# Optimization experiments

Hardware: AMD Instinct MI355X
Metric: run time of the kernel (lower is better)

The kernel has to match this reference:

```python
import jax, jax.numpy as jnp
import numpy as np

DIM = 1024
SCALE = DIM ** (-0.5)
TEMPERATURE = 1.0


def setup_inputs() -> dict:
    key = jax.random.key(0)
    ks = jax.random.split(key, 7)
    B, N, D = 8, 4096, DIM
    s = 1.0 / np.sqrt(D)
    return {
        "x": jax.random.normal(ks[0], (B, N, D), dtype=jnp.float32),
        "Wq": jax.random.normal(ks[1], (D, D), dtype=jnp.float32) * s,
        "bq": jax.random.normal(ks[2], (D,), dtype=jnp.float32) * 0.01,
        "Wk": jax.random.normal(ks[3], (D, D), dtype=jnp.float32) * s,
        "bk": jax.random.normal(ks[4], (D,), dtype=jnp.float32) * 0.01,
        "Wv": jax.random.normal(ks[5], (D, D), dtype=jnp.float32) * s,
        "bv": jax.random.normal(ks[6], (D,), dtype=jnp.float32) * 0.01,
    }


def reference(x, Wq, bq, Wk, bk, Wv, bv):
    B, N, D = x.shape
    # adaptive_avg_pool1d from N -> N//2 with N even == mean over adjacent pairs
    q_input = x.reshape(B, N // 2, 2, D).mean(axis=2)  # [B, N/2, D]
    # torch Linear: y = x @ W.T + b
    q = jnp.einsum("bmd,ed->bme", q_input, Wq) + bq      # [B, N/2, D]
    k = jnp.einsum("bnd,ed->bne", x, Wk) + bk            # [B, N, D]
    v = jnp.einsum("bnd,ed->bne", x, Wv) + bv            # [B, N, D]
    attn = jnp.einsum("bmd,bnd->bmn", q, k) * SCALE      # [B, N/2, N]
    attn = jax.nn.softmax(attn * TEMPERATURE, axis=-1)
    k_out = jnp.einsum("bmn,bnd->bmd", attn, v)          # [B, N/2, D]
    return (q, k_out, k_out)
```

## Files before the change

kernel.cpp:

```cpp
#include <hip/hip_runtime.h>
#include <hip/hip_bf16.h>
#include <cstddef>

typedef __attribute__((ext_vector_type(8))) short s16x8;
typedef __attribute__((ext_vector_type(4))) short s16x4;
typedef __attribute__((ext_vector_type(4))) float f32x4;

#define MFMA_BF16(a, b, c) __builtin_amdgcn_mfma_f32_16x16x32_bf16((a), (b), (c), 0, 0, 0)

__device__ __forceinline__ short f2bf(float f) {
    union { float f; unsigned u; } cv; cv.f = f;
    unsigned u = cv.u;
    unsigned r = (u + 0x7FFFu + ((u >> 16) & 1u)) >> 16;
    return (short)r;
}
__device__ __forceinline__ float bf2f(unsigned short u) {
    union { unsigned u; float f; } cv; cv.u = ((unsigned)u) << 16; return cv.f;
}

__device__ __forceinline__ void gl16(const void* g, void* l) {
    __builtin_amdgcn_global_load_lds(
        (const __attribute__((address_space(1))) void*)g,
        (__attribute__((address_space(3))) void*)l, 16, 0, 0);
}

template <int MODE>
__global__ __launch_bounds__(256, 2) void gemm_bf(
    const void* __restrict__ Ap, const short* __restrict__ Bp,
    const float* __restrict__ bias, const float* __restrict__ lvec,
    void* __restrict__ Cp, void* __restrict__ Cp2,
    int zbase, float* __restrict__ lpart)
{
    constexpr int NT  = (MODE == 4 || MODE == 7) ? 64 : 16;
    constexpr int LDA = (MODE == 4 || MODE == 7) ? 4096 : 1024;
    constexpr int LDB = (MODE == 4 || MODE == 7) ? 4096 : 1024;

    __shared__ short As[128 * 64];
    __shared__ short Bs[128 * 64];
    const int tid = threadIdx.x;

    int bx, by, z;
    if constexpr (MODE == 6 || MODE == 7) {
        const int n = blockIdx.x;
        z = (n & 3) + zbase; const int m = n >> 2; by = m % 16; bx = m / 16;
    } else if constexpr (MODE == 1 || MODE == 3 || MODE == 4 || MODE == 5) {
        const int n = blockIdx.x;
        constexpr int NBY = (MODE == 1) ? 8 : 16;
        z = n & 7; const int m = n >> 3; by = m % NBY; bx = m / NBY;
    } else { bx = blockIdx.x; by = blockIdx.y; z = blockIdx.z; }

    const int w = tid >> 6, l = tid & 63, l15 = l & 15, lhi = l >> 4;
    const int wy = w >> 1, wx = w & 1;
    const int X = (l15 & 7) << 3;
    const int lr8 = l >> 3, cb = l & 7, scb = cb ^ lr8;

    size_t arow0 = (size_t)by * 128, brow0 = (size_t)bx * 128;
    if constexpr (MODE == 3 || MODE == 4 || MODE == 5 || MODE == 6) arow0 += (size_t)z * 2048;
    if constexpr (MODE == 7) arow0 += (size_t)(z & 3) * 2048;
    if constexpr (MODE == 1 || MODE == 3 || MODE == 5 || MODE == 6) brow0 += (size_t)z * 4096;
    if constexpr (MODE == 4 || MODE == 7) brow0 += (size_t)z * 1024;

    const short* Ab = (const short*)Ap;
    const float* Af = (const float*)Ap;

    const short* gA = Ab + (arow0 + w * 32 + lr8) * (size_t)LDA + scb * 8;
    const short* gB = Bp + (brow0 + w * 32 + lr8) * (size_t)LDB + scb * 8;

    f32x4 acc[4][4];
    #pragma unroll
    for (int m = 0; m < 4; ++m)
        #pragma unroll
        for (int n = 0; n < 4; ++n) acc[m][n] = (f32x4){0.f, 0.f, 0.f, 0.f};

    const int r0b = tid >> 3, cb8 = (tid & 7) * 8;
    const int r0f = tid >> 4, kcs = tid & 15;

    for (int kt = 0; kt < NT; ++kt) {
        #pragma unroll
        for (int i = 0; i < 4; ++i)
            gl16(gB + (size_t)(i * 8) * LDB + kt * 64, &Bs[(w * 32 + i * 8) * 64]);
        if constexpr (MODE == 2) {
            #pragma unroll
            for (int p = 0; p < 4; ++p) {
                const int r = r0b + p * 32;
                const size_t g = (arow0 + r) * 2048 + kt * 64 + cb8;
                s16x8 u0 = *(const s16x8*)(Ab + g);
                s16x8 u1 = *(const s16x8*)(Ab + g + 1024);
                s16x8 o;
                #pragma unroll
                for (int j = 0; j < 8; ++j)
                    o[j] = f2bf(0.5f * (bf2f((unsigned short)u0[j]) + bf2f((unsigned short)u1[j])));
                *(s16x8*)&As[r * 64 + (cb8 ^ ((r & 7) * 8))] = o;
            }
        } else if constexpr (MODE == 3) {
            const int k0 = kt * 64 + kcs * 4;
            #pragma unroll
            for (int p = 0; p < 8; ++p) {
                const int r = r0f + p * 16;
                float4 u = *(const float4*)(Af + (arow0 + r) * 1024 + k0);
                s16x4 sa = { f2bf(u.x * 0.03125f), f2bf(u.y * 0.03125f),
                             f2bf(u.z * 0.03125f), f2bf(u.w * 0.03125f) };
                *(s16x4*)&As[r * 64 + ((kcs * 4) ^ ((r & 7) * 8))] = sa;
            }
        } else {
            #pragma unroll
            for (int i = 0; i < 4; ++i)
                gl16(gA + (size_t)(i * 8) * LDA + kt * 64, &As[(w * 32 + i * 8) * 64]);
        }
        __syncthreads();
        #pragma unroll
        for (int kk = 0; kk < 2; ++kk) {
            const int e = (kk * 32 + lhi * 8) ^ X;
            s16x8 af[4], bfr[4];
            #pragma unroll
            for (int m = 0; m < 4; ++m)
                af[m] = *(const s16x8*)&As[(wy * 64 + m * 16 + l15) * 64 + e];
            #pragma unroll
            for (int n = 0; n < 4; ++n)
                bfr[n] = *(const s16x8*)&Bs[(wx * 64 + n * 16 + l15) * 64 + e];
            #pragma unroll
            for (int m = 0; m < 4; ++m)
                #pragma unroll
                for (int n = 0; n < 4; ++n)
                    acc[m][n] = MFMA_BF16(af[m], bfr[n], acc[m][n]);
        }
        __syncthreads();
    }

    #pragma unroll
    for (int m = 0; m < 4; ++m) {
        #pragma unroll
        for (int j = 0; j < 4; ++j) {
            const int rl = wy * 64 + m * 16 + lhi * 4 + j;
            const int grow = by * 128 + rl;
            float radd = 0.f, rmul = 1.f;
            if constexpr (MODE == 1) radd = bias[grow];
            if constexpr (MODE == 4 || MODE == 7) rmul = 1.0f / lvec[(size_t)z * 2048 + grow];
            if constexpr (MODE == 6) {
                float s = 0.f;
                #pragma unroll
                for (int n = 0; n < 4; ++n) {
                    const int gcol = bx * 128 + wx * 64 + n * 16 + l15;
                    const float pv = __expf(acc[m][n][j]);
                    s += pv;
                    ((short*)Cp)[(size_t)(z & 3) * 8388608 + (size_t)grow * 4096 + gcol] = f2bf(pv);
                }
                s += __shfl_xor(s, 1);
                s += __shfl_xor(s, 2);
                s += __shfl_xor(s, 4);
                s += __shfl_xor(s, 8);
                if (l15 == 0)
                    lpart[((size_t)(z & 3) * 2048 + grow) * 64 + bx * 2 + wx] = s;
            } else {
                #pragma unroll
                for (int n = 0; n < 4; ++n) {
                    const int cl = wx * 64 + n * 16 + l15;
                    const int gcol = bx * 128 + cl;
                    float v = acc[m][n][j];
                    if constexpr (MODE == 0) {
                        ((short*)Cp)[(size_t)grow * 1024 + gcol] = f2bf(v + bias[gcol]);
                    } else if constexpr (MODE == 1) {
                        ((short*)Cp)[(size_t)z * 4194304 + (size_t)grow * 4096 + gcol] = f2bf(v + radd);
                    } else if constexpr (MODE == 2) {
                        const float qv = v + bias[gcol];
                        ((float*)Cp)[(size_t)grow * 1024 + gcol] = qv;
                        if (Cp2 != nullptr)
                            ((short*)Cp2)[(size_t)grow * 1024 + gcol] = f2bf(qv * 0.03125f);
                    } else if constexpr (MODE == 3 || MODE == 5) {
                        ((short*)Cp)[(size_t)z * 8388608 + (size_t)grow * 4096 + gcol] = f2bf(v);
                    } else {
                        const size_t o = ((size_t)z * 2048 + grow) * 1024 + gcol;
                        const float ov = v * rmul;
                        ((float*)Cp)[o] = ov;
                        ((float*)Cp2)[o] = ov;
                    }
                }
            }
        }
    }
}

__global__ __launch_bounds__(256, 4) void reduce_l(
    const float* __restrict__ lpart, float* __restrict__ lvec, int zbase)
{
    const int r = blockIdx.x * 256 + threadIdx.x;
    const float4* p = (const float4*)(lpart + (size_t)r * 64);
    float s = 0.f;
    #pragma unroll
    for (int i = 0; i < 16; ++i) { float4 v = p[i]; s += v.x + v.y + v.z + v.w; }
    lvec[(size_t)zbase * 2048 + r] = s;
}

template <int MODE>
__global__ __launch_bounds__(256, 2) void gemm_f32(
    const float* __restrict__ Ap, const float* __restrict__ Bp,
    const float* __restrict__ bias, void* __restrict__ Cp, void* __restrict__ Cp2)
{
    constexpr int LDA = (MODE == 2) ? 2048 : 1024;
    __shared__ short As[128 * 64];
    __shared__ short Bs[128 * 64];
    const int tid = threadIdx.x;
    const int bx = blockIdx.x, by = blockIdx.y, z = blockIdx.z;
    const int w = tid >> 6, l = tid & 63, l15 = l & 15, lhi = l >> 4;
    const int wy = w >> 1, wx = w & 1;
    const int X = (l15 & 7) << 3;

    size_t arow0 = (size_t)by * 128, brow0 = (size_t)bx * 128;
    if constexpr (MODE == 1) brow0 += (size_t)z * 4096;

    f32x4 acc[4][4];
    #pragma unroll
    for (int m = 0; m < 4; ++m)
        #pragma unroll
        for (int n = 0; n < 4; ++n) acc[m][n] = (f32x4){0.f, 0.f, 0.f, 0.f};

    const int r0f = tid >> 4, kcs = tid & 15;
    float4 ra[8], ra2[8], rb[8];

    auto load_tile = [&](int kt) {
        const int k0 = kt * 64 + kcs * 4;
        #pragma unroll
        for (int p = 0; p < 8; ++p) {
            const int r = r0f + p * 16;
            if constexpr (MODE == 2) {
                const float* s0 = Ap + (arow0 + r) * (size_t)LDA + k0;
                ra[p] = *(const float4*)s0;
                ra2[p] = *(const float4*)(s0 + 1024);
            } else {
                ra[p] = *(const float4*)(Ap + (arow0 + r) * (size_t)LDA + k0);
            }
            rb[p] = *(const float4*)(Bp + (brow0 + r) * (size_t)1024 + k0);
        }
    };

    load_tile(0);
    for (int kt = 0; kt < 16; ++kt) {
        #pragma unroll
        for (int p = 0; p < 8; ++p) {
            const int r = r0f + p * 16;
            const int e = (kcs * 4) ^ ((r & 7) << 3);
            float ax, ay, az, aw;
            if constexpr (MODE == 2) {
                ax = 0.5f * (ra[p].x + ra2[p].x); ay = 0.5f * (ra[p].y + ra2[p].y);
                az = 0.5f * (ra[p].z + ra2[p].z); aw = 0.5f * (ra[p].w + ra2[p].w);
            } else {
                ax = ra[p].x; ay = ra[p].y; az = ra[p].z; aw = ra[p].w;
            }
            s16x4 sa = { f2bf(ax), f2bf(ay), f2bf(az), f2bf(aw) };
            *(s16x4*)&As[r * 64 + e] = sa;
            s16x4 sb = { f2bf(rb[p].x), f2bf(rb[p].y), f2bf(rb[p].z), f2bf(rb[p].w) };
            *(s16x4*)&Bs[r * 64 + e] = sb;
        }
        if (kt + 1 < 16) load_tile(kt + 1);
        __syncthreads();
        #pragma unroll
        for (int kk = 0; kk < 2; ++kk) {
            const int e = (kk * 32 + lhi * 8) ^ X;
            s16x8 af[4], bfr[4];
            #pragma unroll
            for (int m = 0; m < 4; ++m)
                af[m] = *(const s16x8*)&As[(wy * 64 + m * 16 + l15) * 64 + e];
            #pragma unroll
            for (int n = 0; n < 4; ++n)
                bfr[n] = *(const s16x8*)&Bs[(wx * 64 + n * 16 + l15) * 64 + e];
            #pragma unroll
            for (int m = 0; m < 4; ++m)
                #pragma unroll
                for (int n = 0; n < 4; ++n)
                    acc[m][n] = MFMA_BF16(af[m], bfr[n], acc[m][n]);
        }
        __syncthreads();
    }

    #pragma unroll
    for (int m = 0; m < 4; ++m) {
        #pragma unroll
        for (int j = 0; j < 4; ++j) {
            const int rl = wy * 64 + m * 16 + lhi * 4 + j;
            const int grow = by * 128 + rl;
            const float radd = (MODE == 1) ? bias[grow] : 0.f;
            #pragma unroll
            for (int n = 0; n < 4; ++n) {
                const int cl = wx * 64 + n * 16 + l15;
                const int gcol = bx * 128 + cl;
                float v = acc[m][n][j];
                if constexpr (MODE == 0) {
                    ((short*)Cp)[(size_t)grow * 1024 + gcol] = f2bf(v + bias[gcol]);
                } else if constexpr (MODE == 1) {
                    ((short*)Cp)[(size_t)z * 4194304 + (size_t)grow * 4096 + gcol] = f2bf(v + radd);
                } else {
                    const float q = v + bias[gcol];
                    ((float*)Cp)[(size_t)grow * 1024 + gcol] = q;
                    ((short*)Cp2)[(size_t)grow * 1024 + gcol] = f2bf(q * 0.03125f);
                }
            }
        }
    }
}

__global__ __launch_bounds__(256, 4) void convert_x(const float* __restrict__ x,
                                                    short* __restrict__ xb)
{
    const size_t i0 = ((size_t)blockIdx.x * 256 + threadIdx.x) * 8;
    float4 a = *(const float4*)(x + i0), b = *(const float4*)(x + i0 + 4);
    s16x8 o = { f2bf(a.x), f2bf(a.y), f2bf(a.z), f2bf(a.w),
                f2bf(b.x), f2bf(b.y), f2bf(b.z), f2bf(b.w) };
    *(s16x8*)(xb + i0) = o;
}

__global__ __launch_bounds__(256, 4) void convert_w(
    const float* __restrict__ Wq, const float* __restrict__ Wk,
    const float* __restrict__ Wv, short* __restrict__ Wb)
{
    const int gid = blockIdx.x * 256 + threadIdx.x;
    const int seg = gid >> 17;
    const size_t off = (size_t)(gid & 131071) * 8;
    const float* s = (seg == 0) ? Wq : ((seg == 1) ? Wk : Wv);
    float4 a = *(const float4*)(s + off), b = *(const float4*)(s + off + 4);
    s16x8 o = { f2bf(a.x), f2bf(a.y), f2bf(a.z), f2bf(a.w),
                f2bf(b.x), f2bf(b.y), f2bf(b.z), f2bf(b.w) };
    *(s16x8*)(Wb + (size_t)seg * 1048576 + off) = o;
}

__global__ __launch_bounds__(256, 4) void softmax_rows(
    const unsigned short* __restrict__ Sin, unsigned short* __restrict__ Pout,
    float* __restrict__ lvec)
{
    const int w = threadIdx.x >> 6, l = threadIdx.x & 63;
    const int row = blockIdx.x * 4 + w;
    const unsigned short* rp = Sin + (size_t)row * 4096;
    unsigned short* wp = Pout + (size_t)row * 4096;

    s16x8 v[8];
    #pragma unroll
    for (int c = 0; c < 8; ++c)
        v[c] = *(const s16x8*)(rp + (c * 64 + l) * 8);

    float mx = -1e30f;
    #pragma unroll
    for (int c = 0; c < 8; ++c)
        #pragma unroll
        for (int j = 0; j < 8; ++j)
            mx = fmaxf(mx, bf2f((unsigned short)v[c][j]));
    #pragma unroll
    for (int d = 1; d < 64; d <<= 1) mx = fmaxf(mx, __shfl_xor(mx, d));

    float sum = 0.f;
    #pragma unroll
    for (int c = 0; c < 8; ++c) {
        #pragma unroll
        for (int j = 0; j < 8; ++j) {
            const float p = __expf(bf2f((unsigned short)v[c][j]) - mx);
            sum += p;
            v[c][j] = f2bf(p);
        }
    }
    #pragma unroll
    for (int d = 1; d < 64; d <<= 1) sum += __shfl_xor(sum, d);

    #pragma unroll
    for (int c = 0; c < 8; ++c)
        *(s16x8*)(wp + (c * 64 + l) * 8) = v[c];
    if (l == 0) lvec[row] = sum;
}

__global__ __launch_bounds__(256, 4) void dup_out(
    const float4* __restrict__ O, float4* __restrict__ o1, float4* __restrict__ o2)
{
    const size_t i0 = (size_t)blockIdx.x * 256 + threadIdx.x;
    #pragma unroll
    for (int p = 0; p < 4; ++p) {
        const size_t i = i0 + (size_t)p * 1048576;
        const float4 t = O[i];
        o1[i] = t;
        o2[i] = t;
    }
}

extern "C" void kernel_launch(void* const* d_in, const int* in_sizes, int n_in,
                              void* d_out, int out_size, void* d_ws, size_t ws_size,
                              hipStream_t stream) {
    const float* x  = (const float*)d_in[0];
    const float* Wq = (const float*)d_in[1];
    const float* bq = (const float*)d_in[2];
    const float* Wk = (const float*)d_in[3];
    const float* bk = (const float*)d_in[4];
    const float* Wv = (const float*)d_in[5];
    const float* bv = (const float*)d_in[6];

    float* out   = (float*)d_out;
    float* q_out = out;
    float* out1  = out + (size_t)16777216;
    float* out2  = out + (size_t)33554432;
    short* Smat  = (short*)out1;

    const unsigned long long NEED_A2 = 241434624ULL;
    const unsigned long long NEED_A1 = 207683584ULL;

    if ((unsigned long long)ws_size >= NEED_A2) {
        short* xb  = (short*)d_ws;
        short* Wb  = xb + (size_t)33554432;
        short* kws = Wb + (size_t)3145728;
        short* vT  = kws + (size_t)33554432;
        short* qs  = vT + (size_t)33554432;
        float* lws = (float*)(qs + (size_t)16777216);
        short* Pws   = (short*)d_ws;
        float* lpart = (float*)((char*)d_ws + 67108864);

        convert_x<<<dim3(16384, 1, 1), 256, 0, stream>>>(x, xb);
        convert_w<<<dim3(1536, 1, 1), 256, 0, stream>>>(Wq, Wk, Wv, Wb);
        gemm_bf<0><<<dim3(8, 256, 1), 256, 0, stream>>>(xb, Wb + 1048576, bk, nullptr, (void*)kws, nullptr, 0, nullptr);
        gemm_bf<1><<<dim3(2048, 1, 1), 256, 0, stream>>>(Wb + 2097152, xb, bv, nullptr, (void*)vT, nullptr, 0, nullptr);
        gemm_bf<2><<<dim3(8, 128, 1), 256, 0, stream>>>(xb, Wb, bq, nullptr, (void*)q_out, (void*)qs, 0, nullptr);
        for (int half = 0; half < 2; ++half) {
            const int zb = half * 4;
            gemm_bf<6><<<dim3(2048, 1, 1), 256, 0, stream>>>(qs, kws, nullptr, nullptr, (void*)Pws, nullptr, zb, lpart);
            reduce_l<<<dim3(32, 1, 1), 256, 0, stream>>>(lpart, lws, zb);
            gemm_bf<7><<<dim3(512, 1, 1), 256, 0, stream>>>(Pws, vT, nullptr, lws, (void*)out1, (void*)out2, zb, nullptr);
        }
    } else if ((unsigned long long)ws_size >= NEED_A1) {
        short* xb  = (short*)d_ws;
        short* Wb  = xb + (size_t)33554432;
        short* kws = Wb + (size_t)3145728;
        short* vT  = kws + (size_t)33554432;
        float* lws = (float*)((char*)d_ws + 207618048ULL);
        unsigned short* Pws = (unsigned short*)d_ws;

        convert_x<<<dim3(16384, 1, 1), 256, 0, stream>>>(x, xb);
        convert_w<<<dim3(1536, 1, 1), 256, 0, stream>>>(Wq, Wk, Wv, Wb);
        gemm_bf<0><<<dim3(8, 256, 1), 256, 0, stream>>>(xb, Wb + 1048576, bk, nullptr, (void*)kws, nullptr, 0, nullptr);
        gemm_bf<1><<<dim3(2048, 1, 1), 256, 0, stream>>>(Wb + 2097152, xb, bv, nullptr, (void*)vT, nullptr, 0, nullptr);
        gemm_bf<2><<<dim3(8, 128, 1), 256, 0, stream>>>(xb, Wb, bq, nullptr, (void*)q_out, nullptr, 0, nullptr);
        gemm_bf<3><<<dim3(4096, 1, 1), 256, 0, stream>>>(q_out, kws, nullptr, nullptr, (void*)Smat, nullptr, 0, nullptr);
        softmax_rows<<<dim3(4096, 1, 1), 256, 0, stream>>>((const unsigned short*)Smat, Pws, lws);
        gemm_bf<4><<<dim3(1024, 1, 1), 256, 0, stream>>>(Pws, vT, nullptr, lws, (void*)out1, (void*)out2, 0, nullptr);
    } else {
        short* kws = (short*)d_ws;
        short* vT  = kws + (size_t)33554432;
        short* qs  = vT + (size_t)33554432;
        float* lws = (float*)((char*)d_ws + 167772160ULL);
        float* Ows = (float*)d_ws;

        gemm_f32<0><<<dim3(8, 256, 1), 256, 0, stream>>>(x, Wk, bk, (void*)kws, nullptr);
        gemm_f32<1><<<dim3(32, 8, 8), 256, 0, stream>>>(Wv, x, bv, (void*)vT, nullptr);
        gemm_f32<2><<<dim3(8, 128, 1), 256, 0, stream>>>(x, Wq, bq, (void*)q_out, (void*)qs);
        gemm_bf<5><<<dim3(4096, 1, 1), 256, 0, stream>>>(qs, kws, nullptr, nullptr, (void*)Smat, nullptr, 0, nullptr);
        softmax_rows<<<dim3(4096, 1, 1), 256, 0, stream>>>((const unsigned short*)Smat, (unsigned short*)Smat, lws);
        gemm_bf<4><<<dim3(1024, 1, 1), 256, 0, stream>>>(Smat, vT, nullptr, lws, (void*)Ows, (void*)Ows, 0, nullptr);
        dup_out<<<dim3(4096, 1, 1), 256, 0, stream>>>((const float4*)Ows, (float4*)out1, (float4*)out2);
    }
}
```

Measured before the change: 636.9 us.

## Add 256x256-tile double-buffered QK^T kernel with exp epilogue

Replaces the 128x128-tile QK^T+exp GEMM with a new 512-thread kernel computing 256x256 output tiles, double-buffered LDS staging via global_load_lds, and fragment reuse across four MFMA sub-phases with setprio. Larger tiles raise arithmetic intensity and cut global traffic per FLOP for the score matrix. The cost is heavy LDS use (128KB) and many accumulator registers, which may limit occupancy. The lpart layout must still match what reduce_l expects (64 partials per row).

```diff
diff --git a/kernel.cpp b/kernel.cpp
--- a/kernel.cpp
+++ b/kernel.cpp
@@ -22,6 +22,166 @@
     __builtin_amdgcn_global_load_lds(
         (const __attribute__((address_space(1))) void*)g,
         (__attribute__((address_space(3))) void*)l, 16, 0, 0);
+}
+
+template <int MODE>
+__global__ __launch_bounds__(512, 2) void g256(
+    const short* __restrict__ Ap, const short* __restrict__ Bp,
+    void* __restrict__ Cp, int zbase, float* __restrict__ lpart)
+{
+    constexpr int NT = 16;
+    constexpr int LDA = 1024, LDB = 1024;
+
+    __shared__ short As[2][16384];
+    __shared__ short Bs[2][16384];
+
+    const int tid = threadIdx.x;
+    const int n = blockIdx.x;
+    const int z = (n & 3) + zbase;
+    const int m_ = n >> 2;
+    const int by = m_ & 7, bx = m_ >> 3;
+    const int w = tid >> 6, l = tid & 63, l15 = l & 15, lhi = l >> 4;
+    const int wr = w >> 2, wc = w & 3;
+    const int X = (l15 & 7) << 3;
+    const int lr8 = l >> 3, cb = l & 7, scb = cb ^ lr8;
+
+    const size_t arow0 = (size_t)z * 2048 + (size_t)by * 256;
+    const size_t brow0 = (size_t)z * 4096 + (size_t)bx * 256;
+
+    const short* gA = Ap + (arow0 + w * 8 + lr8) * (size_t)LDA + scb * 8;
+    const short* gB = Bp + (brow0 + w * 8 + lr8) * (size_t)LDB + scb * 8;
+
+    f32x4 acc[8][4];
+    #pragma unroll
+    for (int mm = 0; mm < 8; ++mm)
+        #pragma unroll
+        for (int nn = 0; nn < 4; ++nn) acc[mm][nn] = (f32x4){0.f, 0.f, 0.f, 0.f};
+
+    auto STAGE = [&](int c, int t) {
+        #pragma unroll
+        for (int i = 0; i < 4; ++i)
+            gl16(gA + (size_t)(i * 64) * LDA + t * 64, &As[c][(i * 64 + w * 8) * 64]);
+        #pragma unroll
+        for (int i = 0; i < 4; ++i)
+            gl16(gB + (size_t)(i * 64) * LDB + t * 64, &Bs[c][(i * 64 + w * 8) * 64]);
+    };
+
+    STAGE(0, 0);
+    asm volatile("s_waitcnt vmcnt(0)" ::: "memory");
+    __builtin_amdgcn_s_barrier();
+
+    s16x8 a[4][2], b[2][2];
+
+    for (int t = 0; t < NT; ++t) {
+        const int c = t & 1;
+        const short* Ab = &As[c][0];
+        const short* Bb = &Bs[c][0];
+
+        #pragma unroll
+        for (int mm = 0; mm < 4; ++mm)
+            #pragma unroll
+            for (int kk = 0; kk < 2; ++kk)
+                a[mm][kk] = *(const s16x8*)&Ab[(wr * 128 + mm * 16 + l15) * 64 + ((kk * 32 + lhi * 8) ^ X)];
+        #pragma unroll
+        for (int nn = 0; nn < 2; ++nn)
+            #pragma unroll
+            for (int kk = 0; kk < 2; ++kk)
+                b[nn][kk] = *(const s16x8*)&Bb[(wc * 64 + nn * 16 + l15) * 64 + ((kk * 32 + lhi * 8) ^ X)];
+        if (t + 1 < NT) STAGE(c ^ 1, t + 1);
+        __builtin_amdgcn_s_barrier();
+        asm volatile("s_waitcnt lgkmcnt(0)" ::: "memory");
+        __builtin_amdgcn_sched_barrier(0);
+        __builtin_amdgcn_s_setprio(1);
+        #pragma unroll
+        for (int mm = 0; mm < 4; ++mm)
+            #pragma unroll
+            for (int nn = 0; nn < 2; ++nn)
+                #pragma unroll
+                for (int kk = 0; kk < 2; ++kk)
+                    acc[mm][nn] = MFMA_BF16(a[mm][kk], b[nn][kk], acc[mm][nn]);
+        __builtin_amdgcn_s_setprio(0);
+        __builtin_amdgcn_s_barrier();
+
+        #pragma unroll
+        for (int nn = 0; nn < 2; ++nn)
+            #pragma unroll
+            for (int kk = 0; kk < 2; ++kk)
+                b[nn][kk] = *(const s16x8*)&Bb[(wc * 64 + (2 + nn) * 16 + l15) * 64 + ((kk * 32 + lhi * 8) ^ X)];
+        __builtin_amdgcn_s_barrier();
+        asm volatile("s_waitcnt lgkmcnt(0)" ::: "memory");
+        __builtin_amdgcn_sched_barrier(0);
+        __builtin_amdgcn_s_setprio(1);
+        #pragma unroll
+        for (int mm = 0; mm < 4; ++mm)
+            #pragma unroll
+            for (int nn = 0; nn < 2; ++nn)
+                #pragma unroll
+                for (int kk = 0; kk < 2; ++kk)
+                    acc[mm][2 + nn] = MFMA_BF16(a[mm][kk], b[nn][kk], acc[mm][2 + nn]);
+        __builtin_amdgcn_s_setprio(0);
+        __builtin_amdgcn_s_barrier();
+
+        #pragma unroll
+        for (int mm = 0; mm < 4; ++mm)
+            #pragma unroll
+            for (int kk = 0; kk < 2; ++kk)
+                a[mm][kk] = *(const s16x8*)&Ab[(wr * 128 + (4 + mm) * 16 + l15) * 64 + ((kk * 32 + lhi * 8) ^ X)];
+        __builtin_amdgcn_s_barrier();
+        asm volatile("s_waitcnt lgkmcnt(0)" ::: "memory");
+        __builtin_amdgcn_sched_barrier(0);
+        __builtin_amdgcn_s_setprio(1);
+        #pragma unroll
+        for (int mm = 0; mm < 4; ++mm)
+            #pragma unroll
+            for (int nn = 0; nn < 2; ++nn)
+                #pragma unroll
+                for (int kk = 0; kk < 2; ++kk)
+                    acc[4 + mm][2 + nn] = MFMA_BF16(a[mm][kk], b[nn][kk], acc[4 + mm][2 + nn]);
+        __builtin_amdgcn_s_setprio(0);
+        __builtin_amdgcn_s_barrier();
+
+        #pragma unroll
+        for (int nn = 0; nn < 2; ++nn)
+            #pragma unroll
+            for (int kk = 0; kk < 2; ++kk)
+                b[nn][kk] = *(const s16x8*)&Bb[(wc * 64 + nn * 16 + l15) * 64 + ((kk * 32 + lhi * 8) ^ X)];
+        __builtin_amdgcn_s_barrier();
+        asm volatile("s_waitcnt lgkmcnt(0)" ::: "memory");
+        __builtin_amdgcn_sched_barrier(0);
+        __builtin_amdgcn_s_setprio(1);
+        #pragma unroll
+        for (int mm = 0; mm < 4; ++mm)
+            #pragma unroll
+            for (int nn = 0; nn < 2; ++nn)
+                #pragma unroll
+                for (int kk = 0; kk < 2; ++kk)
+                    acc[4 + mm][nn] = MFMA_BF16(a[mm][kk], b[nn][kk], acc[4 + mm][nn]);
+        __builtin_amdgcn_s_setprio(0);
+        asm volatile("s_waitcnt vmcnt(0)" ::: "memory");
+        __builtin_amdgcn_s_barrier();
+    }
+
+    #pragma unroll
+    for (int mm = 0; mm < 8; ++mm) {
+        #pragma unroll
+        for (int j = 0; j < 4; ++j) {
+            const int gr = by * 256 + wr * 128 + mm * 16 + lhi * 4 + j;
+            float s = 0.f;
+            #pragma unroll
+            for (int nn = 0; nn < 4; ++nn) {
+                const int gc = bx * 256 + wc * 64 + nn * 16 + l15;
+                const float pv = __expf(acc[mm][nn][j]);
+                s += pv;
+                ((short*)Cp)[(size_t)(z & 3) * 8388608 + (size_t)gr * 4096 + gc] = f2bf(pv);
+            }
+            s += __shfl_xor(s, 1);
+            s += __shfl_xor(s, 2);
+            s += __shfl_xor(s, 4);
+            s += __shfl_xor(s, 8);
+            if (l15 == 0)
+                lpart[((size_t)(z & 3) * 2048 + gr) * 64 + bx * 4 + wc] = s;
+        }
+    }
 }
 
 template <int MODE>
@@ -414,7 +574,7 @@
         gemm_bf<2><<<dim3(8, 128, 1), 256, 0, stream>>>(xb, Wb, bq, nullptr, (void*)q_out, (void*)qs, 0, nullptr);
         for (int half = 0; half < 2; ++half) {
             const int zb = half * 4;
-            gemm_bf<6><<<dim3(2048, 1, 1), 256, 0, stream>>>(qs, kws, nullptr, nullptr, (void*)Pws, nullptr, zb, lpart);
+            g256<6><<<dim3(512, 1, 1), 512, 0, stream>>>(qs, kws, (void*)Pws, zb, lpart);
             reduce_l<<<dim3(32, 1, 1), 256, 0, stream>>>(lpart, lws, zb);
             gemm_bf<7><<<dim3(512, 1, 1), 256, 0, stream>>>(Pws, vT, nullptr, lws, (void*)out1, (void*)out2, zb, nullptr);
         }
```

Measured after the change: 665.3 us. +4.4%, slower.
